# Kernel optimization log

Hardware: AMD Instinct MI355X
Metric: run time of the kernel (lower is better)

## Reference

```python
import jax, jax.numpy as jnp
import numpy as np

B, H, S, D = 1, 16, 4096, 64

def setup_inputs() -> dict:
    key = jax.random.key(0)
    kq, kk, kv = jax.random.split(key, 3)
    q = jax.random.normal(kq, (B, H, S, D), dtype=jnp.float32)
    k = jax.random.normal(kk, (B, H, S, D), dtype=jnp.float32)
    v = jax.random.normal(kv, (B, H, S, D), dtype=jnp.float32)
    # causal mask, broadcastable over batch and heads: True = attend
    mask = jnp.tril(jnp.ones((S, S), dtype=bool))[None, None, :, :]
    return {"q": q, "k": k, "v": v, "mask": mask}


def reference(q, k, v, mask):
    # Chunked attention in the original is mathematically identical to full
    # attention: each query-chunk softmaxes over ALL keys. Vectorized form:
    dim_head = q.shape[-1]
    scale = 1.0 / jnp.sqrt(jnp.asarray(dim_head, dtype=q.dtype))
    scores = jnp.einsum("bhqd,bhkd->bhqk", q, k) * scale  # [B,H,S,S]
    scores = jnp.where(mask, scores, -jnp.inf)
    attn = jax.nn.softmax(scores, axis=-1)
    attn = jnp.nan_to_num(attn, nan=0.0)  # rows with all keys masked -> 0
    return jnp.einsum("bhqk,bhkd->bhqd", attn, v)
```

## Files before the change

### kernel.cpp

```cpp
#include <hip/hip_runtime.h>
#include <hip/hip_bf16.h>
#include <math.h>


typedef __bf16 bf16;
typedef __bf16 bf16x8 __attribute__((ext_vector_type(8)));
typedef float f32x16 __attribute__((ext_vector_type(16)));

#define NH 16
#define SEQ 4096
#define DH 64
#define QB 128
#define WQ 32
#define KB 64
#define NJ 32
#define LOG2E 1.44269504088896340736f

static __device__ __forceinline__ void mfma32(f32x16& c, bf16x8 a, bf16x8 b) {
  asm("v_mfma_f32_32x32x16_bf16 %0, %1, %2, %0" : "+v"(c) : "v"(a), "v"(b));
}
static __device__ __forceinline__ float exp2a(float x) {
  float r; asm("v_exp_f32 %0, %1" : "=v"(r) : "v"(x)); return r;
}
static __device__ __forceinline__ unsigned pk(float lo, float hi) {
  unsigned r; asm("v_cvt_pk_bf16_f32 %0, %1, %2" : "=v"(r) : "v"(lo), "v"(hi)); return r;
}
static __device__ __forceinline__ void swap32(unsigned& a, unsigned& b) {
  asm("v_permlane32_swap_b32 %0, %1" : "+v"(a), "+v"(b));
}

union AFrag { unsigned u[4]; bf16x8 v; };

static __device__ __forceinline__ bf16x8 cvt8(float4 a, float4 b) {
  bf16x8 f;
  f[0]=(bf16)a.x; f[1]=(bf16)a.y; f[2]=(bf16)a.z; f[3]=(bf16)a.w;
  f[4]=(bf16)b.x; f[5]=(bf16)b.y; f[6]=(bf16)b.z; f[7]=(bf16)b.w;
  return f;
}

__global__ void zero_ctr(unsigned* c) { if (threadIdx.x == 0) *c = 0; }


__global__ __launch_bounds__(256, 3)
void fa_fwd(const float* __restrict__ Q, const float* __restrict__ K,
            const float* __restrict__ V, float* __restrict__ O,
            void* __restrict__ ws, const int nitems, const int Lt,
            const int nslot) {
  __shared__ bf16 Ksh[2][KB * DH];
  __shared__ bf16 Vts[2][DH * KB];
  __shared__ int sh_item;

  unsigned* ctr = (unsigned*)ws;
  bf16*  wsO = (bf16*)((char*)ws + 256);
  float* wsM = (float*)((char*)ws + 256 + (size_t)nslot * 16384);
  float* wsL = wsM + (size_t)nslot * 128;

  const int tid = threadIdx.x;
  const int w   = tid >> 6;
  const int l   = tid & 63;
  const int lc  = l & 31;
  const int hi  = l >> 5;

  const int kr = tid >> 2, kc = (tid & 3) * 16;
  const int dg = tid & 7,  kp = tid >> 3;

  for (;;) {
    __syncthreads();
    if (tid == 0) sh_item = (int)atomicAdd(ctr, 1u);
    __syncthreads();
    const int c = sh_item;
    if (c >= nitems) break;

    int j = 0, ci = 0, head = 0, sbase = 0, nc = 1;
    {
      int cc = c;
      for (int jj = NJ - 1; jj >= 0; --jj) {
        const int ncj = (2 * jj + 2 + Lt - 1) / Lt;
        const int cnt = ncj * NH;
        if (cc < cnt) { j = jj; nc = ncj; ci = cc >> 4; head = cc & 15; break; }
        cc -= cnt;
        if (ncj > 1) sbase += ncj;
      }
    }
    const int qb = j * QB;
    const int t0 = ci * Lt;
    const int t1 = min((ci + 1) * Lt, 2 * j + 2);
    const int slot = (nc > 1) ? (sbase + ci) * NH + head : -1;

    const int qw = qb + w * WQ;
    const int qv = qw + lc;
    const float* Qh = Q + (size_t)head * SEQ * DH;
    const float* Kh = K + (size_t)head * SEQ * DH;
    const float* Vh = V + (size_t)head * SEQ * DH;

    bf16x8 qf[4];
    {
      const float* qp = Qh + (size_t)qv * DH + hi * 8;
      const float sc = 0.125f * LOG2E;
#pragma unroll
      for (int ch = 0; ch < 4; ++ch) {
        float4 x = *(const float4*)(qp + ch * 16);
        float4 y = *(const float4*)(qp + ch * 16 + 4);
        bf16x8 f;
        f[0]=(bf16)(x.x*sc); f[1]=(bf16)(x.y*sc); f[2]=(bf16)(x.z*sc); f[3]=(bf16)(x.w*sc);
        f[4]=(bf16)(y.x*sc); f[5]=(bf16)(y.y*sc); f[6]=(bf16)(y.z*sc); f[7]=(bf16)(y.w*sc);
        qf[ch] = f;
      }
    }

    f32x16 o0 = {}, o1 = {};
    float m = -INFINITY, ls = 0.f;

    float4 kreg[4], vreg[4];
    {
      const int kb0 = t0 * KB;
      const float* p = Kh + (size_t)(kb0 + kr) * DH + kc;
#pragma unroll
      for (int i = 0; i < 4; ++i) kreg[i] = ((const float4*)p)[i];
      const float* pv = Vh + (size_t)(kb0 + 2 * kp) * DH + dg * 8;
      vreg[0] = ((const float4*)pv)[0];
      vreg[1] = ((const float4*)pv)[1];
      vreg[2] = ((const float4*)(pv + DH))[0];
      vreg[3] = ((const float4*)(pv + DH))[1];
    }

    for (int t = t0; t < t1; ++t) {
      const int kb = t * KB;
      const int b  = (t - t0) & 1;

      {
        const int Sk = (((kr & 7) ^ ((kr >> 3) & 7)) << 4);
#pragma unroll
        for (int q = 0; q < 2; ++q)
          *(bf16x8*)((char*)Ksh[b] + kr * 128 + ((kc * 2 + q * 16) ^ Sk)) =
              cvt8(kreg[2*q], kreg[2*q+1]);
        const int xbase = (kp * 4) ^ (dg << 4);
#pragma unroll
        for (int i = 0; i < 8; ++i) {
          const float lo = vreg[(i >> 2)    ][i & 3];
          const float hv = vreg[(i >> 2) + 2][i & 3];
          *(unsigned*)((char*)Vts[b] + (dg * 8 + i) * 128 + (xbase ^ (i << 4))) =
              pk(lo, hv);
        }
      }
      __syncthreads();

      if (t + 1 < t1) {
        const int kn = kb + KB;
        const float* p = Kh + (size_t)(kn + kr) * DH + kc;
#pragma unroll
        for (int i = 0; i < 4; ++i) kreg[i] = ((const float4*)p)[i];
        const float* pv = Vh + (size_t)(kn + 2 * kp) * DH + dg * 8;
        vreg[0] = ((const float4*)pv)[0];
        vreg[1] = ((const float4*)pv)[1];
        vreg[2] = ((const float4*)(pv + DH))[0];
        vreg[3] = ((const float4*)(pv + DH))[1];
      }

      if (kb > qw + 31) continue;

      f32x16 st0 = {}, st1 = {};
#pragma unroll
      for (int kt = 0; kt < 2; ++kt) {
        const int row = kt * 32 + lc;
        const int Sr  = (((lc & 7) ^ ((kt * 4 + (lc >> 3)) & 7)) << 4);
        f32x16& st = kt ? st1 : st0;
#pragma unroll
        for (int ch = 0; ch < 4; ++ch) {
          const bf16x8 kf = *(const bf16x8*)((const char*)Ksh[b] +
              row * 128 + ((ch * 32 + hi * 16) ^ Sr));
          mfma32(st, kf, qf[ch]);
        }
      }

      if (kb + 63 > qw) {
#pragma unroll
        for (int r = 0; r < 16; ++r) {
          const int kg = kb + ((r & 3) + 8 * (r >> 2) + 4 * hi);
          if (kg > qv)      st0[r] = -INFINITY;
          if (kg + 32 > qv) st1[r] = -INFINITY;
        }
      }

      float acc[8];
#pragma unroll
      for (int i = 0; i < 8; ++i)
        acc[i] = fmaxf(fmaxf(st0[i], st0[i + 8]), fmaxf(st1[i], st1[i + 8]));
      acc[0]=fmaxf(acc[0],acc[4]); acc[1]=fmaxf(acc[1],acc[5]);
      acc[2]=fmaxf(acc[2],acc[6]); acc[3]=fmaxf(acc[3],acc[7]);
      acc[0]=fmaxf(acc[0],acc[2]); acc[1]=fmaxf(acc[1],acc[3]);
      float mx = fmaxf(acc[0], acc[1]);
      mx = fmaxf(mx, __shfl_xor(mx, 32));

      if (__any(mx > m + 8.0f)) {
        const float mn = fmaxf(m, mx);
        const float al = exp2a(m - mn);
        m = mn;
        ls *= al;
#pragma unroll
        for (int r = 0; r < 16; ++r) {
          const float aq = __shfl(al, (r & 3) + 8 * (r >> 2) + 4 * hi);
          o0[r] *= aq; o1[r] *= aq;
        }
      }

      float rs = 0.f;
      const int S0 = (((lc & 7) ^ ((lc >> 3) & 7)) << 4);
      const int S1 = (((lc & 7) ^ (((lc >> 3) + 4) & 7)) << 4);
#pragma unroll
      for (int ks = 0; ks < 4; ++ks) {
        const f32x16& st = (ks < 2) ? st0 : st1;
        float p[8];
#pragma unroll
        for (int jj = 0; jj < 8; ++jj) p[jj] = exp2a(st[(ks & 1) * 8 + jj] - m);
        rs += ((p[0]+p[1])+(p[2]+p[3])) + ((p[4]+p[5])+(p[6]+p[7]));
        unsigned u0 = pk(p[0],p[1]), u1 = pk(p[2],p[3]);
        unsigned u2 = pk(p[4],p[5]), u3 = pk(p[6],p[7]);
        swap32(u0, u2); swap32(u1, u3);
        AFrag af; af.u[0]=u0; af.u[1]=u1; af.u[2]=u2; af.u[3]=u3;
        const int koff = ks * 32 + hi * 16;
        bf16x8 v0 = *(const bf16x8*)((const char*)Vts[b] + lc * 128 + (koff ^ S0));
        bf16x8 v1 = *(const bf16x8*)((const char*)Vts[b] + (lc + 32) * 128 + (koff ^ S1));
        mfma32(o0, af.v, v0);
        mfma32(o1, af.v, v1);
      }
      rs += __shfl_xor(rs, 32);
      ls += rs;
    }

    if (slot < 0) {
      const float inv = 1.0f / ls;
      float* Ob = O + (size_t)(head * SEQ + qw) * DH;
#pragma unroll
      for (int r = 0; r < 16; ++r) {
        const int row = (r & 3) + 8 * (r >> 2) + 4 * hi;
        const float iq = __shfl(inv, row);
        Ob[(size_t)row * DH + lc]      = o0[r] * iq;
        Ob[(size_t)row * DH + 32 + lc] = o1[r] * iq;
      }
    } else {
      bf16* po = wsO + (size_t)slot * (128 * 64);
#pragma unroll
      for (int r = 0; r < 16; ++r) {
        const int row = w * WQ + (r & 3) + 8 * (r >> 2) + 4 * hi;
        po[row * 64 + lc]      = (bf16)o0[r];
        po[row * 64 + 32 + lc] = (bf16)o1[r];
      }
      if (hi == 0) {
        wsM[slot * 128 + w * WQ + lc] = m;
        wsL[slot * 128 + w * WQ + lc] = ls;
      }
    }
  }
}

__global__ __launch_bounds__(256)
void fa_combine(float* __restrict__ O, const void* __restrict__ ws,
                const int Lt, const int nslot) {
  const bf16*  wsO = (const bf16*)((const char*)ws + 256);
  const float* wsM = (const float*)((const char*)ws + 256 + (size_t)nslot * 16384);
  const float* wsL = wsM + (size_t)nslot * 128;

  const int li = blockIdx.x * 256 + threadIdx.x;
  const int dp = li & 7;
  const int r  = li >> 3;
  const int sj = blockIdx.y;
  const int h  = blockIdx.z;

  int j = 0, sbase = 0, nc = 0;
  {
    int cnt = 0;
    for (int jj = NJ - 1; jj >= 0; --jj) {
      const int ncj = (2 * jj + 2 + Lt - 1) / Lt;
      if (ncj > 1) {
        if (cnt == sj) { j = jj; nc = ncj; break; }
        ++cnt; sbase += ncj;
      }
    }
  }

  float M = -INFINITY;
  for (int c = 0; c < nc; ++c)
    M = fmaxf(M, wsM[((sbase + c) * NH + h) * 128 + r]);

  float lt = 0.f, o[8] = {0.f,0.f,0.f,0.f,0.f,0.f,0.f,0.f};
  for (int c = 0; c < nc; ++c) {
    const int slot = (sbase + c) * NH + h;
    const float wgt = exp2f(wsM[slot * 128 + r] - M);
    lt += wgt * wsL[slot * 128 + r];
    const bf16x8 a = *(const bf16x8*)(wsO + (size_t)slot * 8192 + r * 64 + dp * 8);
#pragma unroll
    for (int jj = 0; jj < 8; ++jj) o[jj] += wgt * (float)a[jj];
  }
  const float inv = 1.0f / lt;

  float* out = O + ((size_t)h * SEQ + j * QB + r) * DH + dp * 8;
#pragma unroll
  for (int jj = 0; jj < 8; ++jj) out[jj] = o[jj] * inv;
}

extern "C" void kernel_launch(void* const* d_in, const int* in_sizes, int n_in,
                              void* d_out, int out_size, void* d_ws, size_t ws_size,
                              hipStream_t stream) {
  const float* q = (const float*)d_in[0];
  const float* k = (const float*)d_in[1];
  const float* v = (const float*)d_in[2];
  float* out = (float*)d_out;

  const int cand[4] = {16, 22, 32, 64};
  int Lt = 64, nslot = 0, nitems = 0, nsj = 0;
  for (int ic = 0; ic < 4; ++ic) {
    const int L = cand[ic];
    int sl = 0, it = 0, js = 0;
    for (int j = 0; j < NJ; ++j) {
      const int nc = (2 * j + 2 + L - 1) / L;
      it += nc * NH;
      if (nc > 1) { sl += nc * NH; ++js; }
    }
    const size_t need = 256 + (size_t)sl * (16384 + 512 + 512);
    if (need <= ws_size || L == 64) { Lt = L; nslot = sl; nitems = it; nsj = js; break; }
  }

  zero_ctr<<<1, 64, 0, stream>>>((unsigned*)d_ws);
  fa_fwd<<<1024, 256, 0, stream>>>(q, k, v, out, d_ws, nitems, Lt, nslot);
  if (nsj > 0) fa_combine<<<dim3(4, nsj, NH), 256, 0, stream>>>(out, d_ws, Lt, nslot);
}
```

Baseline: 221.4 us.

## Partition work queues per XCC to localize head K/V in L2

Replaces the single global atomic work counter with eight per-XCC queues. Each queue owns two heads, and a workgroup reads its XCC id from a hardware register so it pulls work for heads whose K/V stay in that XCC's L2, stealing from other queues once its own is empty. Items are reordered by chunk index first, then query block, and a split size of 8 is added as a candidate, which raises parallelism at the cost of more combine work. The risks are extra index-decode loops and the assumption that workgroups spread evenly across the XCCs.

```diff
diff --git a/kernel.cpp b/kernel.cpp
--- a/kernel.cpp
+++ b/kernel.cpp
@@ -38,21 +38,28 @@
   return f;
 }
 
-__global__ void zero_ctr(unsigned* c) { if (threadIdx.x == 0) *c = 0; }
+__global__ void zero_ctr(unsigned* c) {
+  if (threadIdx.x < 8) c[threadIdx.x * 16] = 0;
+}
 
 
 __global__ __launch_bounds__(256, 3)
 void fa_fwd(const float* __restrict__ Q, const float* __restrict__ K,
             const float* __restrict__ V, float* __restrict__ O,
-            void* __restrict__ ws, const int nitems, const int Lt,
-            const int nslot) {
+            void* __restrict__ ws, const int nitems_q, const int Lt,
+            const int nslot, const int hshift) {
   __shared__ bf16 Ksh[2][KB * DH];
   __shared__ bf16 Vts[2][DH * KB];
   __shared__ int sh_item;
 
-  unsigned* ctr = (unsigned*)ws;
-  bf16*  wsO = (bf16*)((char*)ws + 256);
-  float* wsM = (float*)((char*)ws + 256 + (size_t)nslot * 16384);
+  unsigned xcc = 0;
+  if (hshift == 1) asm("s_getreg_b32 %0, hwreg(HW_REG_XCC_ID)" : "=s"(xcc));
+  const int qown = (hshift == 1) ? (int)(xcc & 7) : 0;
+  const int hpq  = 1 << hshift;
+  const int nq   = 16 >> hshift;
+
+  bf16*  wsO = (bf16*)((char*)ws + 1024);
+  float* wsM = (float*)((char*)ws + 1024 + (size_t)nslot * 16384);
   float* wsL = wsM + (size_t)nslot * 128;
 
   const int tid = threadIdx.x;
@@ -64,28 +71,45 @@
   const int kr = tid >> 2, kc = (tid & 3) * 16;
   const int dg = tid & 7,  kp = tid >> 3;
 
+  int qoff = 0;
   for (;;) {
     __syncthreads();
-    if (tid == 0) sh_item = (int)atomicAdd(ctr, 1u);
+    if (tid == 0) sh_item = (int)atomicAdd((unsigned*)ws + (((qown + qoff) % nq) * 16), 1u);
     __syncthreads();
-    const int c = sh_item;
-    if (c >= nitems) break;
-
-    int j = 0, ci = 0, head = 0, sbase = 0, nc = 1;
+    int c = sh_item;
+    if (c >= nitems_q) {
+      if (++qoff >= nq) break;
+      continue;
+    }
+    const int qi = (qown + qoff) % nq;
+
+    const int head = qi + (c & (hpq - 1)) * nq;
+    int j = -1, ci = 0;
     {
-      int cc = c;
-      for (int jj = NJ - 1; jj >= 0; --jj) {
+      int cc = c >> hshift;
+      for (int cic = 0; cic < 8 && j < 0; ++cic) {
+        for (int jj = NJ - 1; jj >= 0; --jj) {
+          const int ncj = (2 * jj + 2 + Lt - 1) / Lt;
+          if (cic < ncj) {
+            if (cc == 0) { j = jj; ci = cic; break; }
+            --cc;
+          }
+        }
+      }
+    }
+    const int ncj_cur = (2 * j + 2 + Lt - 1) / Lt;
+    int slot = -1;
+    if (ncj_cur > 1) {
+      int sb = 0;
+      for (int jj = NJ - 1; jj > j; --jj) {
         const int ncj = (2 * jj + 2 + Lt - 1) / Lt;
-        const int cnt = ncj * NH;
-        if (cc < cnt) { j = jj; nc = ncj; ci = cc >> 4; head = cc & 15; break; }
-        cc -= cnt;
-        if (ncj > 1) sbase += ncj;
-      }
+        if (ncj > 1) sb += ncj;
+      }
+      slot = (sb + ci) * NH + head;
     }
     const int qb = j * QB;
     const int t0 = ci * Lt;
     const int t1 = min((ci + 1) * Lt, 2 * j + 2);
-    const int slot = (nc > 1) ? (sbase + ci) * NH + head : -1;
 
     const int qw = qb + w * WQ;
     const int qv = qw + lc;
@@ -257,8 +281,8 @@
 __global__ __launch_bounds__(256)
 void fa_combine(float* __restrict__ O, const void* __restrict__ ws,
                 const int Lt, const int nslot) {
-  const bf16*  wsO = (const bf16*)((const char*)ws + 256);
-  const float* wsM = (const float*)((const char*)ws + 256 + (size_t)nslot * 16384);
+  const bf16*  wsO = (const bf16*)((const char*)ws + 1024);
+  const float* wsM = (const float*)((const char*)ws + 1024 + (size_t)nslot * 16384);
   const float* wsL = wsM + (size_t)nslot * 128;
 
   const int li = blockIdx.x * 256 + threadIdx.x;
@@ -307,21 +331,23 @@
   const float* v = (const float*)d_in[2];
   float* out = (float*)d_out;
 
-  const int cand[4] = {16, 22, 32, 64};
-  int Lt = 64, nslot = 0, nitems = 0, nsj = 0;
-  for (int ic = 0; ic < 4; ++ic) {
+  const int cand[5] = {8, 16, 22, 32, 64};
+  int Lt = 64, nslot = 0, iph = 0, nsj = 0;
+  for (int ic = 0; ic < 5; ++ic) {
     const int L = cand[ic];
     int sl = 0, it = 0, js = 0;
     for (int j = 0; j < NJ; ++j) {
       const int nc = (2 * j + 2 + L - 1) / L;
-      it += nc * NH;
+      it += nc;
       if (nc > 1) { sl += nc * NH; ++js; }
     }
-    const size_t need = 256 + (size_t)sl * (16384 + 512 + 512);
-    if (need <= ws_size || L == 64) { Lt = L; nslot = sl; nitems = it; nsj = js; break; }
+    const size_t need = 1024 + (size_t)sl * (16384 + 512 + 512);
+    if (need <= ws_size || L == 64) { Lt = L; nslot = sl; iph = it; nsj = js; break; }
   }
+  const int hshift   = (Lt == 64) ? 4 : 1;
+  const int nitems_q = (1 << hshift) * iph;
 
   zero_ctr<<<1, 64, 0, stream>>>((unsigned*)d_ws);
-  fa_fwd<<<1024, 256, 0, stream>>>(q, k, v, out, d_ws, nitems, Lt, nslot);
+  fa_fwd<<<1024, 256, 0, stream>>>(q, k, v, out, d_ws, nitems_q, Lt, nslot, hshift);
   if (nsj > 0) fa_combine<<<dim3(4, nsj, NH), 256, 0, stream>>>(out, d_ws, Lt, nslot);
 }
```

Measured after the change: 241.8 us. 9.2% more time.
